# Kernel tuning notes

Hardware: AMD Instinct MI355X
Metric: run time of the kernel (lower is better)

## Reference

```python
import jax, jax.numpy as jnp
import numpy as np

MAT_MODE = ((0, 1), (0, 2), (1, 2))
VEC_MODE = (2, 1, 0)
DENSITY_SHIFT = -10.0
DISTANCE_SCALE = 25.0


def grid_sample_2d(img, coords):
    # img: [C, H, W]; coords: [N, 2] in [-1, 1], (x indexes W, y indexes H);
    # bilinear, align_corners=True (matches F.grid_sample in the source).
    C, H, W = img.shape
    x = (coords[:, 0] + 1.0) * 0.5 * (W - 1)
    y = (coords[:, 1] + 1.0) * 0.5 * (H - 1)
    x0 = jnp.floor(x)
    y0 = jnp.floor(y)
    wx = x - x0
    wy = y - y0
    x0i = jnp.clip(x0.astype(jnp.int32), 0, W - 1)
    x1i = jnp.clip(x0i + 1, 0, W - 1)
    y0i = jnp.clip(y0.astype(jnp.int32), 0, H - 1)
    y1i = jnp.clip(y0i + 1, 0, H - 1)
    v00 = img[:, y0i, x0i]
    v01 = img[:, y0i, x1i]
    v10 = img[:, y1i, x0i]
    v11 = img[:, y1i, x1i]
    return (v00 * (1 - wx) * (1 - wy) + v01 * wx * (1 - wy)
            + v10 * (1 - wx) * wy + v11 * wx * wy)  # [C, N]


def line_sample_1d(line, t):
    # line: [C, L]; t: [N] in [-1, 1]. Equivalent to the source's grid_sample on a
    # [1, C, L, 1] tensor with coords (0, t): the width dim (size 1) collapses.
    C, L = line.shape
    y = (t + 1.0) * 0.5 * (L - 1)
    y0 = jnp.floor(y)
    wy = y - y0
    y0i = jnp.clip(y0.astype(jnp.int32), 0, L - 1)
    y1i = jnp.clip(y0i + 1, 0, L - 1)
    return line[:, y0i] * (1 - wy) + line[:, y1i] * wy  # [C, N]


def tensorf_features(planes, lines, xyz):
    # planes: [3, C, H, W]; lines: [3, C, L]; xyz: [N, 3] normalized coords.
    # fusion_two='concat' then fusion_one='multiply' == per-plane multiply, concat.
    feats = []
    for i in range(3):
        a, b = MAT_MODE[i]
        pc = jnp.stack([xyz[:, a], xyz[:, b]], axis=-1)  # [N, 2]
        pf = grid_sample_2d(planes[i], pc)               # [C, N]
        lf = line_sample_1d(lines[i], xyz[:, VEC_MODE[i]])  # [C, N]
        feats.append(pf * lf)
    return jnp.concatenate(feats, axis=0)  # [3C, N]


def raw2alpha(sigma, dist):
    # sigma, dist: [Nr, Ns]
    alpha = 1.0 - jnp.exp(-sigma * dist)
    T = jnp.cumprod(jnp.concatenate(
        [jnp.ones((alpha.shape[0], 1), alpha.dtype), 1.0 - alpha + 1e-10], axis=-1), axis=-1)
    weights = alpha * T[:, :-1]
    return alpha, weights, T[:, -1:]


def setup_inputs() -> dict:
    key = jax.random.key(0)
    ks = jax.random.split(key, 10)
    Nr, Ns, G = 4096, 256, 300
    aabb = jnp.array([[-1.5, -1.5, -1.5], [1.5, 1.5, 1.5]], jnp.float32)
    xyz_sampled = jax.random.uniform(ks[0], (Nr, Ns, 3), jnp.float32,
                                     minval=-1.5, maxval=1.5)
    vd = jax.random.normal(ks[1], (Nr, 3), jnp.float32)
    viewdirs = vd / jnp.linalg.norm(vd, axis=-1, keepdims=True)
    near, far = 2.0, 6.0
    t = jnp.linspace(0.0, 1.0, Ns, dtype=jnp.float32)
    z_vals = near * (1.0 - t) + far * t
    z_vals = jnp.broadcast_to(z_vals, (Nr, Ns)) + \
        jax.random.uniform(ks[2], (Nr, Ns), jnp.float32) * ((far - near) / Ns)
    z_vals = jnp.sort(z_vals, axis=-1)
    s = 0.1  # init_scale
    return {
        'xyz_sampled': xyz_sampled,
        'viewdirs': viewdirs,
        'z_vals': z_vals,
        'density_planes': s * jax.random.normal(ks[3], (3, 8, G, G), jnp.float32),
        'density_lines': s * jax.random.normal(ks[4], (3, 8, G), jnp.float32),
        'app_planes': s * jax.random.normal(ks[5], (3, 24, G, G), jnp.float32),
        'app_lines': s * jax.random.normal(ks[6], (3, 24, G), jnp.float32),
        'density_basis_w': jnp.ones((1, 24), jnp.float32),  # source inits to 1/density_dim
        'app_basis_w': s * jax.random.normal(ks[7], (3, 72), jnp.float32),
        'aabb': aabb,
    }


def reference(xyz_sampled, viewdirs, z_vals, density_planes, density_lines,
              app_planes, app_lines, density_basis_w, app_basis_w, aabb):
    Nr, Ns, _ = xyz_sampled.shape
    # normalize_coord: map aabb -> [-1, 1]
    inv_size = 2.0 / (aabb[1] - aabb[0])
    xyz = ((xyz_sampled - aabb[0]) * inv_size - 1.0).reshape(-1, 3)  # [N, 3]

    dfeat = tensorf_features(density_planes, density_lines, xyz)      # [24, N]
    sigma_feat = (density_basis_w @ dfeat).reshape(Nr, Ns)            # basis_mat
    sigma = jax.nn.softplus(sigma_feat + DENSITY_SHIFT)               # fea2denseAct

    # ray-marching distances
    dists = z_vals[:, 1:] - z_vals[:, :-1]
    dists = jnp.concatenate([dists, dists[:, -1:]], axis=-1)
    alpha, weights, bg_T = raw2alpha(sigma, dists * DISTANCE_SCALE)

    # appearance branch: RGBRender is identity on the 3-dim basis output
    afeat = tensorf_features(app_planes, app_lines, xyz)              # [72, N]
    rgb = (app_basis_w @ afeat).T.reshape(Nr, Ns, 3)

    rgb_map = jnp.sum(weights[..., None] * rgb, axis=1)               # [Nr, 3]
    return rgb_map
```

## Files before the change

### kernel.cpp

```cpp
#include <hip/hip_runtime.h>
#include <math.h>

#define G  300
#define NS 256
#define NR 4096
#define CT 32

typedef _Float16 half16_t;
typedef _Float16 h8 __attribute__((ext_vector_type(8)));

__global__ __launch_bounds__(256) void prep_planes(
    const float* __restrict__ dp, const float* __restrict__ ap,
    half16_t* __restrict__ out)
{
  int t = blockIdx.x * blockDim.x + threadIdx.x;
  if (t >= 3 * G * G) return;
  int x  = t % G;
  int yi = t / G;
  int y  = yi % G;
  int i  = yi / G;
  const float* dpp = dp + ((size_t)(i * 8) * G + y) * G + x;
  const float* app = ap + ((size_t)(i * 24) * G + y) * G + x;
  h8 v[4];
#pragma unroll
  for (int c = 0; c < 8; ++c) v[c >> 3][c & 7] = (half16_t)dpp[(size_t)c * G * G];
#pragma unroll
  for (int c = 0; c < 24; ++c) {
    int cc = c + 8;
    v[cc >> 3][cc & 7] = (half16_t)app[(size_t)c * G * G];
  }
  h8* o = (h8*)(out + (size_t)t * CT);
#pragma unroll
  for (int m = 0; m < 4; ++m) o[m] = v[m];
}

__global__ __launch_bounds__(256) void prep_lines(
    const float* __restrict__ dl, const float* __restrict__ al,
    half16_t* __restrict__ out)
{
  int t = blockIdx.x * blockDim.x + threadIdx.x;
  if (t >= 3 * G) return;
  int p = t % G;
  int i = t / G;
  h8 v[4];
#pragma unroll
  for (int c = 0; c < 8; ++c) v[c >> 3][c & 7] = (half16_t)dl[(i * 8 + c) * G + p];
#pragma unroll
  for (int c = 0; c < 24; ++c) {
    int cc = c + 8;
    v[cc >> 3][cc & 7] = (half16_t)al[(i * 24 + c) * G + p];
  }
  h8* o = (h8*)(out + (size_t)t * CT);
#pragma unroll
  for (int m = 0; m < 4; ++m) o[m] = v[m];
}

__global__ __launch_bounds__(256) void tensorf_fused(
    const float* __restrict__ xyz, const float* __restrict__ zv,
    const half16_t* __restrict__ planes, const half16_t* __restrict__ lns,
    const float* __restrict__ dbw, const float* __restrict__ abw,
    const float* __restrict__ aabb, float* __restrict__ out)
{
  __shared__ float4 srgb[4][NS];

  const int wv   = threadIdx.x >> 6;
  const int lane = threadIdx.x & 63;
  const int ray  = (blockIdx.x << 2) + wv;
  const int q    = lane >> 2;
  const int r    = lane & 3;

  float W[3][24];
  if (r == 0) {
#pragma unroll
    for (int m = 0; m < 24; ++m) { W[0][m] = dbw[m]; W[1][m] = 0.f; W[2][m] = 0.f; }
  } else {
#pragma unroll
    for (int j = 0; j < 3; ++j)
#pragma unroll
      for (int i = 0; i < 3; ++i)
#pragma unroll
        for (int k = 0; k < 8; ++k)
          W[j][i * 8 + k] = abw[j * 72 + i * 24 + (r - 1) * 8 + k];
  }

  const float a0x = aabb[0], a0y = aabb[1], a0z = aabb[2];
  const float ivx = 2.f / (aabb[3] - aabb[0]);
  const float ivy = 2.f / (aabb[4] - aabb[1]);
  const float ivz = 2.f / (aabb[5] - aabb[2]);

  const int MA[3] = {0, 0, 1};
  const int MB[3] = {1, 2, 2};
  const int MV[3] = {2, 1, 0};

  const int ro = r * 8;

  for (int it = 0; it < NS / 16; ++it) {
    int s = it * 16 + q;
    const float* xp = xyz + ((size_t)ray * NS + s) * 3;
    float g[3];
    g[0] = (xp[0] - a0x) * ivx - 1.f;
    g[1] = (xp[1] - a0y) * ivy - 1.f;
    g[2] = (xp[2] - a0z) * ivz - 1.f;

    float acc0 = 0.f, acc1 = 0.f, acc2 = 0.f;
#pragma unroll
    for (int i = 0; i < 3; ++i) {
      float fx = (g[MA[i]] + 1.f) * (0.5f * (G - 1));
      float fy = (g[MB[i]] + 1.f) * (0.5f * (G - 1));
      float ft = (g[MV[i]] + 1.f) * (0.5f * (G - 1));
      float x0f = floorf(fx), y0f = floorf(fy), t0f = floorf(ft);
      float wx = fx - x0f, wy = fy - y0f, wt = ft - t0f;
      int x0 = min(max((int)x0f, 0), G - 1);
      int y0 = min(max((int)y0f, 0), G - 1);
      int t0 = min(max((int)t0f, 0), G - 1);
      int x1 = min(x0 + 1, G - 1);
      int y1 = min(y0 + 1, G - 1);
      int t1 = min(t0 + 1, G - 1);

      const half16_t* pb = planes + (size_t)i * G * G * CT;
      h8 t00 = *(const h8*)(pb + ((size_t)(y0 * G + x0)) * CT + ro);
      h8 t01 = *(const h8*)(pb + ((size_t)(y0 * G + x1)) * CT + ro);
      h8 t10 = *(const h8*)(pb + ((size_t)(y1 * G + x0)) * CT + ro);
      h8 t11 = *(const h8*)(pb + ((size_t)(y1 * G + x1)) * CT + ro);
      const half16_t* lb = lns + (size_t)i * G * CT + ro;
      h8 l0 = *(const h8*)(lb + (size_t)t0 * CT);
      h8 l1 = *(const h8*)(lb + (size_t)t1 * CT);

      float w00 = (1.f - wx) * (1.f - wy), w01 = wx * (1.f - wy);
      float w10 = (1.f - wx) * wy,         w11 = wx * wy;
      float wl0 = 1.f - wt;
#pragma unroll
      for (int k = 0; k < 8; ++k) {
        float pf = (float)t00[k] * w00 + (float)t01[k] * w01
                 + (float)t10[k] * w10 + (float)t11[k] * w11;
        float lf = (float)l0[k] * wl0 + (float)l1[k] * wt;
        float f  = pf * lf;
        acc0 += W[0][i * 8 + k] * f;
        acc1 += W[1][i * 8 + k] * f;
        acc2 += W[2][i * 8 + k] * f;
      }
    }
    float4 v;
    v.x = (r == 0) ? acc0 : 0.f;
    v.y = (r == 0) ? 0.f : acc0;
    v.z = (r == 0) ? 0.f : acc1;
    v.w = (r == 0) ? 0.f : acc2;
#pragma unroll
    for (int m = 1; m <= 2; m <<= 1) {
      v.x += __shfl_xor(v.x, m);
      v.y += __shfl_xor(v.y, m);
      v.z += __shfl_xor(v.z, m);
      v.w += __shfl_xor(v.w, m);
    }
    if (r == 0) srgb[wv][s] = v;
  }
  __syncthreads();

  const float* zp = zv + (size_t)ray * NS + lane * 4;
  float4 z4 = *(const float4*)zp;
  float znext = __shfl_down(z4.x, 1);
  float d[4];
  d[0] = z4.y - z4.x;
  d[1] = z4.z - z4.y;
  d[2] = z4.w - z4.z;
  d[3] = (lane == 63) ? d[2] : (znext - z4.w);

  float4 c[4];
  float al[4];
  float tl = 1.f;
#pragma unroll
  for (int j = 0; j < 4; ++j) {
    c[j] = srgb[wv][lane * 4 + j];
    float vs = c[j].x - 10.0f;
    float sp = (vs > 0.f) ? (vs + log1pf(expf(-vs))) : log1pf(expf(vs));
    al[j] = 1.f - expf(-sp * (d[j] * 25.0f));
    tl *= (1.f - al[j] + 1e-10f);
  }
  float incl = tl;
#pragma unroll
  for (int off = 1; off < 64; off <<= 1) {
    float p = __shfl_up(incl, off);
    if (lane >= off) incl *= p;
  }
  float T = __shfl_up(incl, 1);
  if (lane == 0) T = 1.f;

  float ar = 0.f, ag = 0.f, ab = 0.f;
#pragma unroll
  for (int j = 0; j < 4; ++j) {
    float w = al[j] * T;
    ar += w * c[j].y;
    ag += w * c[j].z;
    ab += w * c[j].w;
    T *= (1.f - al[j] + 1e-10f);
  }
#pragma unroll
  for (int off = 32; off > 0; off >>= 1) {
    ar += __shfl_down(ar, off);
    ag += __shfl_down(ag, off);
    ab += __shfl_down(ab, off);
  }
  if (lane == 0) {
    out[ray * 3 + 0] = ar;
    out[ray * 3 + 1] = ag;
    out[ray * 3 + 2] = ab;
  }
}

extern "C" void kernel_launch(void* const* d_in, const int* in_sizes, int n_in,
                              void* d_out, int out_size, void* d_ws, size_t ws_size,
                              hipStream_t stream)
{
  const float* xyz  = (const float*)d_in[0];
  const float* zv   = (const float*)d_in[2];
  const float* dp   = (const float*)d_in[3];
  const float* dl   = (const float*)d_in[4];
  const float* ap   = (const float*)d_in[5];
  const float* al   = (const float*)d_in[6];
  const float* dbw  = (const float*)d_in[7];
  const float* abw  = (const float*)d_in[8];
  const float* aabb = (const float*)d_in[9];
  float* out = (float*)d_out;

  half16_t* planes16 = (half16_t*)d_ws;
  half16_t* lines16  = planes16 + (size_t)3 * G * G * CT;

  hipLaunchKernelGGL(prep_planes, dim3((3 * G * G + 255) / 256), dim3(256), 0, stream,
                     dp, ap, planes16);
  hipLaunchKernelGGL(prep_lines, dim3((3 * G + 255) / 256), dim3(256), 0, stream,
                     dl, al, lines16);
  hipLaunchKernelGGL(tensorf_fused, dim3(NR / 4), dim3(256), 0, stream,
                     xyz, zv, planes16, lines16, dbw, abw, aabb, out);
}
```

Measured before the change: 237.9 us.

## Split fused kernel into gather and scan kernels, widen prep parallelism

The fused per-ray kernel is split into a gather kernel that samples features for a short run of samples per wave and writes float4 results to a workspace buffer, and a separate scan kernel that does the alpha compositing per ray. This exposes many more independent blocks to the gather stage, adds an occupancy hint, and lets it run at higher occupancy without a block-wide barrier. The prep kernels now use four threads per texel, each converting eight channels, to increase parallelism. The cost is an extra round trip of per-sample features through global memory and one more launch.

```diff
diff --git a/kernel.cpp b/kernel.cpp
--- a/kernel.cpp
+++ b/kernel.cpp
@@ -14,24 +14,20 @@
     half16_t* __restrict__ out)
 {
   int t = blockIdx.x * blockDim.x + threadIdx.x;
-  if (t >= 3 * G * G) return;
-  int x  = t % G;
-  int yi = t / G;
+  if (t >= 3 * G * G * 4) return;
+  int m   = t & 3;
+  int tex = t >> 2;
+  int x  = tex % G;
+  int yi = tex / G;
   int y  = yi % G;
   int i  = yi / G;
-  const float* dpp = dp + ((size_t)(i * 8) * G + y) * G + x;
-  const float* app = ap + ((size_t)(i * 24) * G + y) * G + x;
-  h8 v[4];
-#pragma unroll
-  for (int c = 0; c < 8; ++c) v[c >> 3][c & 7] = (half16_t)dpp[(size_t)c * G * G];
-#pragma unroll
-  for (int c = 0; c < 24; ++c) {
-    int cc = c + 8;
-    v[cc >> 3][cc & 7] = (half16_t)app[(size_t)c * G * G];
-  }
-  h8* o = (h8*)(out + (size_t)t * CT);
-#pragma unroll
-  for (int m = 0; m < 4; ++m) o[m] = v[m];
+  const size_t GG = (size_t)G * G;
+  const float* p = (m == 0) ? (dp + (size_t)(i * 8) * GG + (size_t)y * G + x)
+                            : (ap + (size_t)(i * 24 + (m - 1) * 8) * GG + (size_t)y * G + x);
+  h8 v;
+#pragma unroll
+  for (int c = 0; c < 8; ++c) v[c] = (half16_t)p[c * GG];
+  *(h8*)(out + (size_t)tex * CT + m * 8) = v;
 }
 
 __global__ __launch_bounds__(256) void prep_lines(
@@ -39,35 +35,32 @@
     half16_t* __restrict__ out)
 {
   int t = blockIdx.x * blockDim.x + threadIdx.x;
-  if (t >= 3 * G) return;
-  int p = t % G;
-  int i = t / G;
-  h8 v[4];
-#pragma unroll
-  for (int c = 0; c < 8; ++c) v[c >> 3][c & 7] = (half16_t)dl[(i * 8 + c) * G + p];
-#pragma unroll
-  for (int c = 0; c < 24; ++c) {
-    int cc = c + 8;
-    v[cc >> 3][cc & 7] = (half16_t)al[(i * 24 + c) * G + p];
-  }
-  h8* o = (h8*)(out + (size_t)t * CT);
-#pragma unroll
-  for (int m = 0; m < 4; ++m) o[m] = v[m];
-}
-
-__global__ __launch_bounds__(256) void tensorf_fused(
-    const float* __restrict__ xyz, const float* __restrict__ zv,
+  if (t >= 3 * G * 4) return;
+  int m   = t & 3;
+  int tex = t >> 2;
+  int p = tex % G;
+  int i = tex / G;
+  h8 v;
+#pragma unroll
+  for (int c = 0; c < 8; ++c)
+    v[c] = (m == 0) ? (half16_t)dl[(i * 8 + c) * G + p]
+                    : (half16_t)al[(i * 24 + (m - 1) * 8 + c) * G + p];
+  *(h8*)(out + (size_t)tex * CT + m * 8) = v;
+}
+
+#define ITER 4
+
+__global__ __launch_bounds__(256, 4) void tensorf_gather(
+    const float* __restrict__ xyz,
     const half16_t* __restrict__ planes, const half16_t* __restrict__ lns,
     const float* __restrict__ dbw, const float* __restrict__ abw,
-    const float* __restrict__ aabb, float* __restrict__ out)
-{
-  __shared__ float4 srgb[4][NS];
-
+    const float* __restrict__ aabb, float4* __restrict__ feat)
+{
+  const int lane = threadIdx.x & 63;
   const int wv   = threadIdx.x >> 6;
-  const int lane = threadIdx.x & 63;
-  const int ray  = (blockIdx.x << 2) + wv;
   const int q    = lane >> 2;
   const int r    = lane & 3;
+  const int waveId = (blockIdx.x << 2) + wv;
 
   float W[3][24];
   if (r == 0) {
@@ -91,12 +84,12 @@
   const int MA[3] = {0, 0, 1};
   const int MB[3] = {1, 2, 2};
   const int MV[3] = {2, 1, 0};
-
   const int ro = r * 8;
 
-  for (int it = 0; it < NS / 16; ++it) {
-    int s = it * 16 + q;
-    const float* xp = xyz + ((size_t)ray * NS + s) * 3;
+#pragma unroll 1
+  for (int it = 0; it < ITER; ++it) {
+    int s = (waveId * ITER + it) * 16 + q;
+    const float* xp = xyz + (size_t)s * 3;
     float g[3];
     g[0] = (xp[0] - a0x) * ivx - 1.f;
     g[1] = (xp[1] - a0y) * ivy - 1.f;
@@ -152,9 +145,17 @@
       v.z += __shfl_xor(v.z, m);
       v.w += __shfl_xor(v.w, m);
     }
-    if (r == 0) srgb[wv][s] = v;
-  }
-  __syncthreads();
+    if (r == 0) feat[s] = v;
+  }
+}
+
+__global__ __launch_bounds__(256) void tensorf_scan(
+    const float* __restrict__ zv, const float4* __restrict__ feat,
+    float* __restrict__ out)
+{
+  const int wv   = threadIdx.x >> 6;
+  const int lane = threadIdx.x & 63;
+  const int ray  = (blockIdx.x << 2) + wv;
 
   const float* zp = zv + (size_t)ray * NS + lane * 4;
   float4 z4 = *(const float4*)zp;
@@ -170,7 +171,7 @@
   float tl = 1.f;
 #pragma unroll
   for (int j = 0; j < 4; ++j) {
-    c[j] = srgb[wv][lane * 4 + j];
+    c[j] = feat[(size_t)ray * NS + lane * 4 + j];
     float vs = c[j].x - 10.0f;
     float sp = (vs > 0.f) ? (vs + log1pf(expf(-vs))) : log1pf(expf(vs));
     al[j] = 1.f - expf(-sp * (d[j] * 25.0f));
@@ -224,11 +225,14 @@
 
   half16_t* planes16 = (half16_t*)d_ws;
   half16_t* lines16  = planes16 + (size_t)3 * G * G * CT;
-
-  hipLaunchKernelGGL(prep_planes, dim3((3 * G * G + 255) / 256), dim3(256), 0, stream,
+  float4*   feat     = (float4*)(lines16 + (size_t)3 * G * CT);
+
+  hipLaunchKernelGGL(prep_planes, dim3((3 * G * G * 4 + 255) / 256), dim3(256), 0, stream,
                      dp, ap, planes16);
-  hipLaunchKernelGGL(prep_lines, dim3((3 * G + 255) / 256), dim3(256), 0, stream,
+  hipLaunchKernelGGL(prep_lines, dim3((3 * G * 4 + 255) / 256), dim3(256), 0, stream,
                      dl, al, lines16);
-  hipLaunchKernelGGL(tensorf_fused, dim3(NR / 4), dim3(256), 0, stream,
-                     xyz, zv, planes16, lines16, dbw, abw, aabb, out);
-}
+  hipLaunchKernelGGL(tensorf_gather, dim3(NR * NS / (16 * ITER * 4)), dim3(256), 0, stream,
+                     xyz, planes16, lines16, dbw, abw, aabb, feat);
+  hipLaunchKernelGGL(tensorf_scan, dim3(NR / 4), dim3(256), 0, stream,
+                     zv, feat, out);
+}
```

Result: slower. 484.6 us (+103.7%).
